# Performance work log

Measured on AMD Instinct MI355X. Metric: run time of the kernel, lower is better.

## Reference

```python
import jax, jax.numpy as jnp
import numpy as np

B, D, TC, TE, TGT = 8, 256, 2048, 2048, 256
SCALE = 16.0  # sqrt(256.0) hardcoded in the original module


def setup_inputs() -> dict:
    key = jax.random.key(0)
    k1, k2, k3 = jax.random.split(key, 3)
    content_emb = jax.random.normal(k1, (B, D, TC), dtype=jnp.float32)
    emotion_emb = jax.random.normal(k2, (B, D, TE), dtype=jnp.float32)
    # Conv1d(embed_dim*2 -> target_embed, kernel=3): weight [out, in, k]
    fan_in = 2 * D * 3
    conv_w = jax.random.normal(k3, (TGT, 2 * D, 3), dtype=jnp.float32) / np.sqrt(fan_in)
    conv_b = jnp.zeros((TGT,), dtype=jnp.float32)
    return {"content_emb": content_emb, "emotion_emb": emotion_emb,
            "conv_w": conv_w, "conv_b": conv_b}


def reference(content_emb, emotion_emb, conv_w, conv_b):
    # (B, D, T) -> (B, T, D)
    c = jnp.transpose(content_emb, (0, 2, 1))   # [B, Tc, D]
    e = jnp.transpose(emotion_emb, (0, 2, 1))   # [B, Te, D]
    sim = jnp.einsum('btd,bsd->bts', c, e)      # [B, Tc, Te]
    attn = jax.nn.softmax(sim / SCALE, axis=-1)
    weighted_emo = jnp.einsum('bts,bsd->btd', attn, e)  # [B, Tc, D]
    x = jnp.concatenate([c, weighted_emo], axis=-1)     # [B, Tc, 2D]
    x = jnp.transpose(x, (0, 2, 1))                     # [B, 2D, Tc]
    out = jax.lax.conv_general_dilated(
        x, conv_w, window_strides=(1,), padding=[(1, 1)],
        dimension_numbers=('NCH', 'OIH', 'NCH'))
    return out + conv_b[None, :, None]
```

## Files before the change

### kernel.cpp

```cpp
#include <hip/hip_runtime.h>

typedef __bf16 bf16x8 __attribute__((ext_vector_type(8)));
typedef __bf16 bf16x4 __attribute__((ext_vector_type(4)));
typedef float  f32x4  __attribute__((ext_vector_type(4)));

#define MFMA(a, b, c) __builtin_amdgcn_mfma_f32_16x16x32_bf16((a), (b), (c), 0, 0, 0)
#define DRAIN_VMCNT() __builtin_amdgcn_s_waitcnt(0x0F70)

constexpr int Bc  = 8;
constexpr int D   = 256;
constexpr int TC  = 2048;
constexpr int TE  = 2048;
constexpr int TGT = 256;
constexpr int XR  = 512;
constexpr int CROW = 520;
constexpr int NBT = Bc * TC;

__device__ __forceinline__ void gl_lds16(const __bf16* g, __bf16* l) {
  __builtin_amdgcn_global_load_lds(
      (const __attribute__((address_space(1))) void*)g,
      (__attribute__((address_space(3))) void*)l, 16, 0, 0);
}

__global__ void k_transpose_f(const float* __restrict__ src, __bf16* __restrict__ dst,
                              int T, int rowStride) {
  __shared__ __bf16 tile[64][68];
  const int b  = blockIdx.z;
  const int t0 = blockIdx.x * 64;
  const int d0 = blockIdx.y * 64;
  const int tid = threadIdx.x;
  const int c4 = (tid & 15) * 4;
  const int r0 = tid >> 4;
  const float* sp = src + ((size_t)b * D + d0) * T + t0;
#pragma unroll
  for (int i = 0; i < 4; ++i) {
    const int r = r0 + 16 * i;
    const float4 v = *(const float4*)(sp + (size_t)r * T + c4);
    bf16x4 wv;
    wv[0] = (__bf16)v.x; wv[1] = (__bf16)v.y; wv[2] = (__bf16)v.z; wv[3] = (__bf16)v.w;
    *(bf16x4*)&tile[r][c4] = wv;
  }
  __syncthreads();
  const int c = tid & 63, rr0 = tid >> 6;
  __bf16* dp = dst + ((size_t)b * T + t0) * rowStride + d0;
#pragma unroll
  for (int r = rr0; r < 64; r += 4) dp[(size_t)r * rowStride + c] = tile[c][r];
}

__global__ void k_prep_emo(const float* __restrict__ src, __bf16* __restrict__ e_t,
                           __bf16* __restrict__ e_ds) {
  __shared__ __bf16 tile[64][68];
  const int b  = blockIdx.z;
  const int t0 = blockIdx.x * 64;
  const int d0 = blockIdx.y * 64;
  const int tid = threadIdx.x;
  const int c4 = (tid & 15) * 4;
  const int r0 = tid >> 4;
  const float* sp = src + ((size_t)b * D + d0) * TE + t0;
  __bf16* dsp = e_ds + ((size_t)b * D + d0) * TE + t0;
#pragma unroll
  for (int i = 0; i < 4; ++i) {
    const int r = r0 + 16 * i;
    const float4 v = *(const float4*)(sp + (size_t)r * TE + c4);
    bf16x4 wv;
    wv[0] = (__bf16)v.x; wv[1] = (__bf16)v.y; wv[2] = (__bf16)v.z; wv[3] = (__bf16)v.w;
    *(bf16x4*)&tile[r][c4] = wv;
    *(bf16x4*)(dsp + (size_t)r * TE + c4) = wv;
  }
  __syncthreads();
  const int c = tid & 63, rr0 = tid >> 6;
  __bf16* dp = e_t + ((size_t)b * TE + t0) * D + d0;
#pragma unroll
  for (int r = rr0; r < 64; r += 4) dp[(size_t)r * D + c] = tile[c][r];
}

__global__ void k_wpack_f(const float* __restrict__ w, __bf16* __restrict__ Wk) {
  const int idx = blockIdx.x * 256 + threadIdx.x;
  const int o = idx >> 9, i = idx & 511;
#pragma unroll
  for (int k = 0; k < 3; ++k)
    Wk[k * (TGT * 512) + idx] = (__bf16)w[(size_t)o * 1536 + i * 3 + k];
}

__global__ __launch_bounds__(256, 2) void k_attn(const __bf16* __restrict__ xcat,
                                                 const __bf16* __restrict__ e_t,
                                                 const __bf16* __restrict__ e_ds,
                                                 __bf16* __restrict__ Op,
                                                 float* __restrict__ Lp) {
  __shared__ __align__(16) __bf16 sEt[2][8192];
  __shared__ __align__(16) __bf16 sEs[2][8192];
  __shared__ __align__(16) __bf16 sP[4][2][640];

  const int tid  = threadIdx.x;
  const int lane = tid & 63;
  const int w    = tid >> 6;
  const int q    = lane >> 4;
  const int tl   = lane & 15;
  const int b    = blockIdx.y;
  const int z    = blockIdx.z;
  const int tbase = blockIdx.x * 128 + w * 32;

  const __bf16* etb = e_t  + (size_t)b * TE * D;
  const __bf16* esb = e_ds + (size_t)b * D * TE;

  bf16x8 cB[2][8];
#pragma unroll
  for (int tt = 0; tt < 2; ++tt) {
    const __bf16* crow = xcat + ((size_t)(b * TC) + tbase + tt * 16 + tl) * XR + q * 8;
#pragma unroll
    for (int ks = 0; ks < 8; ++ks) cB[tt][ks] = *(const bf16x8*)(crow + ks * 32);
  }

  unsigned offEt[4], offEs[4];
#pragma unroll
  for (int c = 0; c < 4; ++c) {
    const int id = (w * 4 + c) * 64 + lane;
    const int ss = id >> 5, cs = id & 31;
    offEt[c] = ss * D + (cs ^ (ss & 7)) * 8;
    const int dd = id >> 2, ps = id & 3;
    offEs[c] = dd * TE + (ps ^ ((dd >> 2) & 3)) * 8;
  }

  f32x4 accO[2][16];
#pragma unroll
  for (int tt = 0; tt < 2; ++tt)
#pragma unroll
    for (int dt = 0; dt < 16; ++dt) accO[tt][dt] = (f32x4){0.f, 0.f, 0.f, 0.f};
  float lacc[2] = {0.f, 0.f};

  const int sbase = z * (TE / 4);
  const int sw3 = (tl >> 2) & 3;

  auto stage = [&](int buf, int s0) {
#pragma unroll
    for (int c = 0; c < 4; ++c) {
      gl_lds16(etb + (size_t)s0 * D + offEt[c], &sEt[buf][(w * 4 + c) * 512]);
      gl_lds16(esb + s0 + offEs[c], &sEs[buf][(w * 4 + c) * 512]);
    }
  };

  stage(0, sbase);
  DRAIN_VMCNT();
  __syncthreads();

  int cur = 0;
  for (int k = 0; k < TE / 128; ++k) {
    if (k < TE / 128 - 1) stage(cur ^ 1, sbase + (k + 1) * 32);

    f32x4 aS[2][2];
#pragma unroll
    for (int i = 0; i < 2; ++i)
#pragma unroll
      for (int j = 0; j < 2; ++j) aS[i][j] = (f32x4){0.f, 0.f, 0.f, 0.f};
    const __bf16* pe = &sEt[cur][0];
#pragma unroll
    for (int ks = 0; ks < 8; ++ks) {
      const int ch = (ks * 4 + q) ^ (tl & 7);
      bf16x8 a0 = *(const bf16x8*)(pe + (tl * 32 + ch) * 8);
      bf16x8 a1 = *(const bf16x8*)(pe + ((16 + tl) * 32 + ch) * 8);
      aS[0][0] = MFMA(a0, cB[0][ks], aS[0][0]);
      aS[0][1] = MFMA(a0, cB[1][ks], aS[0][1]);
      aS[1][0] = MFMA(a1, cB[0][ks], aS[1][0]);
      aS[1][1] = MFMA(a1, cB[1][ks], aS[1][1]);
    }

#pragma unroll
    for (int tt = 0; tt < 2; ++tt) {
      bf16x4 w0, w1;
#pragma unroll
      for (int r = 0; r < 4; ++r) {
        float e0 = __expf(aS[0][tt][r] * 0.0625f);
        float e1 = __expf(aS[1][tt][r] * 0.0625f);
        lacc[tt] += e0 + e1;
        w0[r] = (__bf16)e0;
        w1[r] = (__bf16)e1;
      }
      __bf16* pw = &sP[w][tt][tl * 40 + q * 4];
      *(bf16x4*)pw = w0;
      *(bf16x4*)(pw + 16) = w1;
    }
    bf16x8 pB0 = *(const bf16x8*)(&sP[w][0][tl * 40 + q * 8]);
    bf16x8 pB1 = *(const bf16x8*)(&sP[w][1][tl * 40 + q * 8]);

    const __bf16* ps = &sEs[cur][0];
#pragma unroll
    for (int dt = 0; dt < 16; ++dt) {
      bf16x8 a = *(const bf16x8*)(ps + ((dt * 16 + tl) * 4 + (q ^ sw3)) * 8);
      accO[0][dt] = MFMA(a, pB0, accO[0][dt]);
      accO[1][dt] = MFMA(a, pB1, accO[1][dt]);
    }

    DRAIN_VMCNT();
    __syncthreads();
    cur ^= 1;
  }

#pragma unroll
  for (int tt = 0; tt < 2; ++tt) {
    float v = lacc[tt];
    v += __shfl_xor(v, 16, 64);
    v += __shfl_xor(v, 32, 64);
    const size_t row = (size_t)z * NBT + b * TC + tbase + tt * 16 + tl;
    if (q == 0) Lp[row] = v;
    __bf16* orow = Op + row * D + q * 4;
#pragma unroll
    for (int dt = 0; dt < 16; ++dt) {
      bf16x4 o;
#pragma unroll
      for (int r = 0; r < 4; ++r) o[r] = (__bf16)accO[tt][dt][r];
      *(bf16x4*)(orow + dt * 16) = o;
    }
  }
}

__global__ void k_norm(const __bf16* __restrict__ Op, const float* __restrict__ Lp,
                       __bf16* __restrict__ xcat) {
  const int row  = blockIdx.x * 4 + (threadIdx.x >> 6);
  const int lane = threadIdx.x & 63;
  float lsum = 0.f;
#pragma unroll
  for (int zz = 0; zz < 4; ++zz) lsum += Lp[zz * NBT + row];
  const float inv = 1.0f / lsum;
  float acc[4] = {0.f, 0.f, 0.f, 0.f};
#pragma unroll
  for (int zz = 0; zz < 4; ++zz) {
    bf16x4 a = *(const bf16x4*)(Op + ((size_t)zz * NBT + row) * D + lane * 4);
#pragma unroll
    for (int r = 0; r < 4; ++r) acc[r] += (float)a[r];
  }
  bf16x4 o;
#pragma unroll
  for (int r = 0; r < 4; ++r) o[r] = (__bf16)(acc[r] * inv);
  *(bf16x4*)(xcat + (size_t)row * XR + D + lane * 4) = o;
}

__global__ __launch_bounds__(256, 2) void k_conv(const __bf16* __restrict__ xcat,
                                                 const __bf16* __restrict__ Wk,
                                                 const float* __restrict__ bias,
                                                 float* __restrict__ out) {
  __shared__ __align__(16) __bf16 sX[34 * CROW];
  __shared__ __align__(16) __bf16 sW[2][8192];
  const int tid  = threadIdx.x;
  const int lane = tid & 63;
  const int wv   = tid >> 6;
  const int q    = lane >> 4;
  const int tl   = lane & 15;
  const int b    = blockIdx.x & 7;
  const int t0   = (blockIdx.x >> 3) * 32;
  const int o0   = wv * 64;
  const int sw3  = (tl >> 2) & 3;

  const __bf16* xb = xcat + (size_t)b * TC * XR;
  for (int r = wv; r < 34; r += 4) {
    int gr = t0 - 1 + r;
    gr = gr < 0 ? 0 : (gr > TC - 1 ? TC - 1 : gr);
    gl_lds16(xb + (size_t)gr * XR + lane * 8, &sX[r * CROW]);
  }

  unsigned offW[4];
#pragma unroll
  for (int c = 0; c < 4; ++c) {
    const int id = (wv * 4 + c) * 64 + lane;
    const int o = id >> 2, ps = id & 3;
    offW[c] = o * 512 + (ps ^ ((o >> 2) & 3)) * 8;
  }
  auto stageW = [&](int buf, int s) {
    const int kk = s >> 4, is = s & 15;
    const __bf16* wb = Wk + (size_t)kk * TGT * 512 + is * 32;
#pragma unroll
    for (int c = 0; c < 4; ++c)
      gl_lds16(wb + offW[c], &sW[buf][(wv * 4 + c) * 512]);
  };
  stageW(0, 0);
  DRAIN_VMCNT();
  __syncthreads();
  if (t0 == 0)       for (int i = tid; i < CROW; i += 256) sX[i] = (__bf16)0.f;
  if (t0 + 32 == TC) for (int i = tid; i < CROW; i += 256) sX[33 * CROW + i] = (__bf16)0.f;
  __syncthreads();

  f32x4 acc[4][2];
#pragma unroll
  for (int mt = 0; mt < 4; ++mt) {
#pragma unroll
    for (int r = 0; r < 4; ++r) {
      const float bv = bias[o0 + mt * 16 + q * 4 + r];
#pragma unroll
      for (int nt = 0; nt < 2; ++nt) acc[mt][nt][r] = bv;
    }
  }

  int cur = 0;
  for (int s = 0; s < 48; ++s) {
    if (s < 47) stageW(cur ^ 1, s + 1);
    const int kk = s >> 4, is = s & 15;
    bf16x8 bfr[2];
#pragma unroll
    for (int nt = 0; nt < 2; ++nt)
      bfr[nt] = *(const bf16x8*)(&sX[(nt * 16 + tl + kk) * CROW + is * 32 + q * 8]);
#pragma unroll
    for (int mt = 0; mt < 4; ++mt) {
      const int o = o0 + mt * 16 + tl;
      bf16x8 af = *(const bf16x8*)(&sW[cur][(o * 4 + (q ^ sw3)) * 8]);
#pragma unroll
      for (int nt = 0; nt < 2; ++nt) acc[mt][nt] = MFMA(af, bfr[nt], acc[mt][nt]);
    }
    DRAIN_VMCNT();
    __syncthreads();
    cur ^= 1;
  }

#pragma unroll
  for (int mt = 0; mt < 4; ++mt) {
#pragma unroll
    for (int nt = 0; nt < 2; ++nt) {
#pragma unroll
      for (int r = 0; r < 4; ++r) {
        const int o = o0 + mt * 16 + q * 4 + r;
        const int t = t0 + nt * 16 + tl;
        out[((size_t)b * TGT + o) * TC + t] = acc[mt][nt][r];
      }
    }
  }
}

extern "C" void kernel_launch(void* const* d_in, const int* in_sizes, int n_in,
                              void* d_out, int out_size, void* d_ws, size_t ws_size,
                              hipStream_t stream) {
  (void)in_sizes; (void)n_in; (void)out_size; (void)ws_size;
  const float* content = (const float*)d_in[0];
  const float* emotion = (const float*)d_in[1];
  const float* conv_w  = (const float*)d_in[2];
  const float* conv_b  = (const float*)d_in[3];
  float* out = (float*)d_out;

  char* ws = (char*)d_ws;
  __bf16* xcat = (__bf16*)ws;
  __bf16* Wk   = (__bf16*)(ws + 16777216);
  __bf16* Op   = (__bf16*)(ws + 17563648);
  float*  Lp   = (float*)(ws + 51118080);
  __bf16* e_t  = (__bf16*)d_out;
  __bf16* e_ds = (__bf16*)((char*)d_out + 8388608);

  k_transpose_f<<<dim3(TC / 64, D / 64, Bc), 256, 0, stream>>>(content, xcat, TC, XR);
  k_prep_emo<<<dim3(TE / 64, D / 64, Bc), 256, 0, stream>>>(emotion, e_t, e_ds);
  k_wpack_f<<<512, 256, 0, stream>>>(conv_w, Wk);
  k_attn<<<dim3(TC / 128, Bc, 4), 256, 0, stream>>>(xcat, e_t, e_ds, Op, Lp);
  k_norm<<<NBT / 4, 256, 0, stream>>>(Op, Lp, xcat);
  k_conv<<<dim3((TC / 32) * Bc), 256, 0, stream>>>(xcat, Wk, conv_b, out);
}
```

Measured before the change: 183.4 us.

## Vectorize transpose stores, use exp2 softmax, and raise wave priority around MFMA loops

The transpose and emotion-prep kernels now gather eight bf16 values from the LDS tile per thread and write them with one 16-byte store, replacing scalar 2-byte stores, to cut global store transactions. The softmax exponent uses exp2f with a pre-folded log2(e)/16 constant in place of __expf with a 1/16 scale. The attention and conv kernels wrap their MFMA loops in s_setprio(1)/s_setprio(0) so waves doing matrix work get scheduling priority over waves issuing loads. The column-wise LDS reads in the transpose may hit bank conflicts, and the priority hints may do little.

```diff
diff --git a/kernel.cpp b/kernel.cpp
--- a/kernel.cpp
+++ b/kernel.cpp
@@ -15,6 +15,8 @@
 constexpr int XR  = 512;
 constexpr int CROW = 520;
 constexpr int NBT = Bc * TC;
+
+#define EXP_C 0.09016844005556021f
 
 __device__ __forceinline__ void gl_lds16(const __bf16* g, __bf16* l) {
   __builtin_amdgcn_global_load_lds(
@@ -41,10 +43,17 @@
     *(bf16x4*)&tile[r][c4] = wv;
   }
   __syncthreads();
-  const int c = tid & 63, rr0 = tid >> 6;
   __bf16* dp = dst + ((size_t)b * T + t0) * rowStride + d0;
 #pragma unroll
-  for (int r = rr0; r < 64; r += 4) dp[(size_t)r * rowStride + c] = tile[c][r];
+  for (int i = 0; i < 2; ++i) {
+    const int idx = tid + 256 * i;
+    const int r   = idx >> 3;
+    const int c8  = (idx & 7) * 8;
+    bf16x8 v;
+#pragma unroll
+    for (int j = 0; j < 8; ++j) v[j] = tile[c8 + j][r];
+    *(bf16x8*)(dp + (size_t)r * rowStride + c8) = v;
+  }
 }
 
 __global__ void k_prep_emo(const float* __restrict__ src, __bf16* __restrict__ e_t,
@@ -68,10 +77,17 @@
     *(bf16x4*)(dsp + (size_t)r * TE + c4) = wv;
   }
   __syncthreads();
-  const int c = tid & 63, rr0 = tid >> 6;
   __bf16* dp = e_t + ((size_t)b * TE + t0) * D + d0;
 #pragma unroll
-  for (int r = rr0; r < 64; r += 4) dp[(size_t)r * D + c] = tile[c][r];
+  for (int i = 0; i < 2; ++i) {
+    const int idx = tid + 256 * i;
+    const int r   = idx >> 3;
+    const int c8  = (idx & 7) * 8;
+    bf16x8 v;
+#pragma unroll
+    for (int j = 0; j < 8; ++j) v[j] = tile[c8 + j][r];
+    *(bf16x8*)(dp + (size_t)r * D + c8) = v;
+  }
 }
 
 __global__ void k_wpack_f(const float* __restrict__ w, __bf16* __restrict__ Wk) {
@@ -153,6 +169,7 @@
 #pragma unroll
       for (int j = 0; j < 2; ++j) aS[i][j] = (f32x4){0.f, 0.f, 0.f, 0.f};
     const __bf16* pe = &sEt[cur][0];
+    __builtin_amdgcn_s_setprio(1);
 #pragma unroll
     for (int ks = 0; ks < 8; ++ks) {
       const int ch = (ks * 4 + q) ^ (tl & 7);
@@ -163,14 +180,15 @@
       aS[1][0] = MFMA(a1, cB[0][ks], aS[1][0]);
       aS[1][1] = MFMA(a1, cB[1][ks], aS[1][1]);
     }
+    __builtin_amdgcn_s_setprio(0);
 
 #pragma unroll
     for (int tt = 0; tt < 2; ++tt) {
       bf16x4 w0, w1;
 #pragma unroll
       for (int r = 0; r < 4; ++r) {
-        float e0 = __expf(aS[0][tt][r] * 0.0625f);
-        float e1 = __expf(aS[1][tt][r] * 0.0625f);
+        float e0 = exp2f(aS[0][tt][r] * EXP_C);
+        float e1 = exp2f(aS[1][tt][r] * EXP_C);
         lacc[tt] += e0 + e1;
         w0[r] = (__bf16)e0;
         w1[r] = (__bf16)e1;
@@ -183,12 +201,14 @@
     bf16x8 pB1 = *(const bf16x8*)(&sP[w][1][tl * 40 + q * 8]);
 
     const __bf16* ps = &sEs[cur][0];
+    __builtin_amdgcn_s_setprio(1);
 #pragma unroll
     for (int dt = 0; dt < 16; ++dt) {
       bf16x8 a = *(const bf16x8*)(ps + ((dt * 16 + tl) * 4 + (q ^ sw3)) * 8);
       accO[0][dt] = MFMA(a, pB0, accO[0][dt]);
       accO[1][dt] = MFMA(a, pB1, accO[1][dt]);
     }
+    __builtin_amdgcn_s_setprio(0);
 
     DRAIN_VMCNT();
     __syncthreads();
@@ -297,6 +317,7 @@
 #pragma unroll
     for (int nt = 0; nt < 2; ++nt)
       bfr[nt] = *(const bf16x8*)(&sX[(nt * 16 + tl + kk) * CROW + is * 32 + q * 8]);
+    __builtin_amdgcn_s_setprio(1);
 #pragma unroll
     for (int mt = 0; mt < 4; ++mt) {
       const int o = o0 + mt * 16 + tl;
@@ -304,6 +325,7 @@
 #pragma unroll
       for (int nt = 0; nt < 2; ++nt) acc[mt][nt] = MFMA(af, bfr[nt], acc[mt][nt]);
     }
+    __builtin_amdgcn_s_setprio(0);
     DRAIN_VMCNT();
     __syncthreads();
     cur ^= 1;
```

New measurement: 185.9 us. No clear change (+1.4%).
